# Optimization experiments

Measured on AMD Instinct MI355X. Metric: run time of the kernel, lower is better.

## Reference

```python
import jax, jax.numpy as jnp
import numpy as np

B = 2_000_000   # batch of affine transforms
N = 3           # spatial ndims -> flattened transform has N*(N+1)=12 entries


def setup_inputs() -> dict:
    key = jax.random.key(0)
    # small shifts so that identity + shift is always invertible
    trf = jax.random.normal(key, (B, N * (N + 1)), dtype=jnp.float32) * 0.1
    return {"trf": trf}


def reference(trf):
    """Batched equivalent of tf.map_fn(_single_invert, trf).

    Per sample: lift flattened (N,N+1) shift to an (N+1,N+1) matrix over the
    identity, invert it, and convert back to a flattened shift.
    """
    b = trf.shape[0]
    eye = jnp.eye(N + 1, dtype=trf.dtype)
    # affine_shift_to_identity: (b, N, N+1) -> pad zero row -> add identity
    mat = trf.reshape(b, N, N + 1)
    full = jnp.concatenate(
        [mat, jnp.zeros((b, 1, N + 1), dtype=trf.dtype)], axis=1
    ) + eye                                  # (b, N+1, N+1)
    inv = jnp.linalg.inv(full)               # batched tiny inversions
    # affine_identity_to_shift: subtract identity, drop last row, flatten
    shift = (inv - eye)[:, :N, :]            # (b, N, N+1)
    return shift.reshape(b, N * (N + 1))
```

## Files before the change

kernel.cpp:

```cpp
#include <hip/hip_runtime.h>


typedef float nfloat4 __attribute__((ext_vector_type(4)));

__global__ __launch_bounds__(256, 6) void invert_affine_kernel(
    const float4* __restrict__ in, float4* __restrict__ out, int b) {
  __shared__ float4 buf[4][384];

  const int wave = threadIdx.x >> 6;
  const int lane = threadIdx.x & 63;
  float4* wbuf = buf[wave];

  const int s0 = blockIdx.x * 512 + wave * 128;
  const int base_f4 = s0 * 3;
  const int n_f4 = b * 3;

#pragma unroll
  for (int k = 0; k < 6; ++k) {
    const int idx = base_f4 + k * 64 + lane;
    if (idx < n_f4) {
      nfloat4 nv = __builtin_nontemporal_load((const nfloat4*)&in[idx]);
      wbuf[k * 64 + lane] = make_float4(nv.x, nv.y, nv.z, nv.w);
    }
  }
  __builtin_amdgcn_wave_barrier();

#pragma unroll
  for (int si = 0; si < 2; ++si) {
    const int s = s0 + si * 64 + lane;
    if (s < b) {
      const int o = (si * 64 + lane) * 3;
      float4 r0 = wbuf[o + 0];
      float4 r1 = wbuf[o + 1];
      float4 r2 = wbuf[o + 2];

      float a00 = r0.x + 1.0f, a01 = r0.y,        a02 = r0.z,        t0 = r0.w;
      float a10 = r1.x,        a11 = r1.y + 1.0f, a12 = r1.z,        t1 = r1.w;
      float a20 = r2.x,        a21 = r2.y,        a22 = r2.z + 1.0f, t2 = r2.w;

      float b00 = a11 * a22 - a12 * a21;
      float b01 = a02 * a21 - a01 * a22;
      float b02 = a01 * a12 - a02 * a11;
      float b10 = a12 * a20 - a10 * a22;
      float b11 = a00 * a22 - a02 * a20;
      float b12 = a02 * a10 - a00 * a12;
      float b20 = a10 * a21 - a11 * a20;
      float b21 = a01 * a20 - a00 * a21;
      float b22 = a00 * a11 - a01 * a10;

      float det = a00 * b00 + a01 * b10 + a02 * b20;
      float rdet = 1.0f / det;

      b00 *= rdet; b01 *= rdet; b02 *= rdet;
      b10 *= rdet; b11 *= rdet; b12 *= rdet;
      b20 *= rdet; b21 *= rdet; b22 *= rdet;

      wbuf[o + 0] = make_float4(b00 - 1.0f, b01, b02,
                                -(b00 * t0 + b01 * t1 + b02 * t2));
      wbuf[o + 1] = make_float4(b10, b11 - 1.0f, b12,
                                -(b10 * t0 + b11 * t1 + b12 * t2));
      wbuf[o + 2] = make_float4(b20, b21, b22 - 1.0f,
                                -(b20 * t0 + b21 * t1 + b22 * t2));
    }
  }
  __builtin_amdgcn_wave_barrier();

#pragma unroll
  for (int k = 0; k < 6; ++k) {
    const int idx = base_f4 + k * 64 + lane;
    if (idx < n_f4) {
      const float4 vv = wbuf[k * 64 + lane];
      nfloat4 nv;
      nv.x = vv.x; nv.y = vv.y; nv.z = vv.z; nv.w = vv.w;
      __builtin_nontemporal_store(nv, (nfloat4*)&out[idx]);
    }
  }
}

extern "C" void kernel_launch(void* const* d_in, const int* in_sizes, int n_in,
                              void* d_out, int out_size, void* d_ws, size_t ws_size,
                              hipStream_t stream) {
  const float4* trf = (const float4*)d_in[0];
  float4* out = (float4*)d_out;
  int b = in_sizes[0] / 12;
  const int threads = 256;
  const int samples_per_block = 512;
  int blocks = (b + samples_per_block - 1) / samples_per_block;
  invert_affine_kernel<<<blocks, threads, 0, stream>>>(trf, out, b);
}
```

Before: 159.7 us.

## Use persistent grid-stride blocks with register prefetch of next tile

Replaces the one-shot-per-block kernel with a persistent grid of at most 2048 blocks. Each block strides over 256-sample tiles and prefetches the next tile's input into registers while the current tile is computed and stored. Shared memory per block is halved and launch bounds raised to 8 blocks per SIMD to overlap loads with compute and stores. The cost is loop overhead and a fixed grid size that may leave bandwidth unused if occupancy is lower than expected.

```diff
diff --git a/kernel.cpp b/kernel.cpp
--- a/kernel.cpp
+++ b/kernel.cpp
@@ -3,40 +3,59 @@
 
 typedef float nfloat4 __attribute__((ext_vector_type(4)));
 
-__global__ __launch_bounds__(256, 6) void invert_affine_kernel(
+__global__ __launch_bounds__(256, 8) void invert_affine_kernel(
     const float4* __restrict__ in, float4* __restrict__ out, int b) {
-  __shared__ float4 buf[4][384];
+  __shared__ float4 buf[4][192];
 
   const int wave = threadIdx.x >> 6;
   const int lane = threadIdx.x & 63;
   float4* wbuf = buf[wave];
 
-  const int s0 = blockIdx.x * 512 + wave * 128;
-  const int base_f4 = s0 * 3;
   const int n_f4 = b * 3;
+  const int ntiles = (b + 255) >> 8;
+  const int gstride = (int)gridDim.x;
 
-#pragma unroll
-  for (int k = 0; k < 6; ++k) {
-    const int idx = base_f4 + k * 64 + lane;
-    if (idx < n_f4) {
-      nfloat4 nv = __builtin_nontemporal_load((const nfloat4*)&in[idx]);
-      wbuf[k * 64 + lane] = make_float4(nv.x, nv.y, nv.z, nv.w);
+  int it = (int)blockIdx.x;
+  if (it >= ntiles) return;
+
+  nfloat4 r0 = {0.f, 0.f, 0.f, 0.f}, r1 = r0, r2 = r0;
+  {
+    const int base = (it * 256 + wave * 64) * 3 + lane;
+    if (base < n_f4)
+      r0 = __builtin_nontemporal_load((const nfloat4*)&in[base]);
+    if (base + 64 < n_f4)
+      r1 = __builtin_nontemporal_load((const nfloat4*)&in[base + 64]);
+    if (base + 128 < n_f4)
+      r2 = __builtin_nontemporal_load((const nfloat4*)&in[base + 128]);
+  }
+
+  while (true) {
+    wbuf[lane]       = make_float4(r0.x, r0.y, r0.z, r0.w);
+    wbuf[64 + lane]  = make_float4(r1.x, r1.y, r1.z, r1.w);
+    wbuf[128 + lane] = make_float4(r2.x, r2.y, r2.z, r2.w);
+    __builtin_amdgcn_wave_barrier();
+
+    const int nxt = it + gstride;
+    if (nxt < ntiles) {
+      const int base = (nxt * 256 + wave * 64) * 3 + lane;
+      if (base < n_f4)
+        r0 = __builtin_nontemporal_load((const nfloat4*)&in[base]);
+      if (base + 64 < n_f4)
+        r1 = __builtin_nontemporal_load((const nfloat4*)&in[base + 64]);
+      if (base + 128 < n_f4)
+        r2 = __builtin_nontemporal_load((const nfloat4*)&in[base + 128]);
     }
-  }
-  __builtin_amdgcn_wave_barrier();
 
-#pragma unroll
-  for (int si = 0; si < 2; ++si) {
-    const int s = s0 + si * 64 + lane;
+    const int s = it * 256 + wave * 64 + lane;
     if (s < b) {
-      const int o = (si * 64 + lane) * 3;
-      float4 r0 = wbuf[o + 0];
-      float4 r1 = wbuf[o + 1];
-      float4 r2 = wbuf[o + 2];
+      const int o = lane * 3;
+      float4 q0 = wbuf[o + 0];
+      float4 q1 = wbuf[o + 1];
+      float4 q2 = wbuf[o + 2];
 
-      float a00 = r0.x + 1.0f, a01 = r0.y,        a02 = r0.z,        t0 = r0.w;
-      float a10 = r1.x,        a11 = r1.y + 1.0f, a12 = r1.z,        t1 = r1.w;
-      float a20 = r2.x,        a21 = r2.y,        a22 = r2.z + 1.0f, t2 = r2.w;
+      float a00 = q0.x + 1.0f, a01 = q0.y,        a02 = q0.z,        t0 = q0.w;
+      float a10 = q1.x,        a11 = q1.y + 1.0f, a12 = q1.z,        t1 = q1.w;
+      float a20 = q2.x,        a21 = q2.y,        a22 = q2.z + 1.0f, t2 = q2.w;
 
       float b00 = a11 * a22 - a12 * a21;
       float b01 = a02 * a21 - a01 * a22;
@@ -62,18 +81,30 @@
       wbuf[o + 2] = make_float4(b20, b21, b22 - 1.0f,
                                 -(b20 * t0 + b21 * t1 + b22 * t2));
     }
-  }
-  __builtin_amdgcn_wave_barrier();
+    __builtin_amdgcn_wave_barrier();
 
-#pragma unroll
-  for (int k = 0; k < 6; ++k) {
-    const int idx = base_f4 + k * 64 + lane;
-    if (idx < n_f4) {
-      const float4 vv = wbuf[k * 64 + lane];
-      nfloat4 nv;
-      nv.x = vv.x; nv.y = vv.y; nv.z = vv.z; nv.w = vv.w;
-      __builtin_nontemporal_store(nv, (nfloat4*)&out[idx]);
+    {
+      const int base = (it * 256 + wave * 64) * 3 + lane;
+      if (base < n_f4) {
+        float4 v = wbuf[lane];
+        nfloat4 nv; nv.x = v.x; nv.y = v.y; nv.z = v.z; nv.w = v.w;
+        __builtin_nontemporal_store(nv, (nfloat4*)&out[base]);
+      }
+      if (base + 64 < n_f4) {
+        float4 v = wbuf[64 + lane];
+        nfloat4 nv; nv.x = v.x; nv.y = v.y; nv.z = v.z; nv.w = v.w;
+        __builtin_nontemporal_store(nv, (nfloat4*)&out[base + 64]);
+      }
+      if (base + 128 < n_f4) {
+        float4 v = wbuf[128 + lane];
+        nfloat4 nv; nv.x = v.x; nv.y = v.y; nv.z = v.z; nv.w = v.w;
+        __builtin_nontemporal_store(nv, (nfloat4*)&out[base + 128]);
+      }
     }
+    __builtin_amdgcn_wave_barrier();
+
+    if (nxt >= ntiles) break;
+    it = nxt;
   }
 }
 
@@ -84,7 +115,8 @@
   float4* out = (float4*)d_out;
   int b = in_sizes[0] / 12;
   const int threads = 256;
-  const int samples_per_block = 512;
-  int blocks = (b + samples_per_block - 1) / samples_per_block;
+  int blocks = 2048;
+  const int ntiles = (b + 255) >> 8;
+  if (blocks > ntiles) blocks = ntiles;
   invert_affine_kernel<<<blocks, threads, 0, stream>>>(trf, out, b);
 }
```

Result: no change. 162.0 us (+1.5%).
